# Performance work log

Hardware: AMD Instinct MI355X
Metric: run time of the kernel (lower is better)

## Reference

```python
import jax, jax.numpy as jnp
import numpy as np

XYZ_MIN = np.array([-1.0, -1.0, -1.0], np.float32)
XYZ_MAX = np.array([1.0, 1.0, 1.0], np.float32)
N_SAMPLES = 256
T_NEAR, T_FAR = 0.05, 2.0
ALPHA_INIT = 1e-6
ACT_SHIFT = float(np.log(1.0 / (1.0 - ALPHA_INIT) - 1.0))  # density bias shift
INTERVAL = 0.5  # stepsize * voxel_size_ratio
VIEWBASE_PE = 4


def trilerp(grid, pts):
    """grid: [C, X, Y, Z]; pts: [P, 3] world coords. Returns [P, C]."""
    res = jnp.asarray(grid.shape[1:], dtype=pts.dtype)  # [3]
    ind = (pts - XYZ_MIN) / (XYZ_MAX - XYZ_MIN) * (res - 1.0)
    ind = jnp.clip(ind, 0.0, res - 1.0)
    i0 = jnp.minimum(jnp.floor(ind), res - 2.0).astype(jnp.int32)  # [P,3]
    f = ind - i0.astype(pts.dtype)  # [P,3] fractional offsets
    x0, y0, z0 = i0[:, 0], i0[:, 1], i0[:, 2]
    x1, y1, z1 = x0 + 1, y0 + 1, z0 + 1
    fx, fy, fz = f[:, 0], f[:, 1], f[:, 2]
    gx, gy, gz = 1.0 - fx, 1.0 - fy, 1.0 - fz
    out = (grid[:, x0, y0, z0] * (gx * gy * gz)
           + grid[:, x1, y0, z0] * (fx * gy * gz)
           + grid[:, x0, y1, z0] * (gx * fy * gz)
           + grid[:, x0, y0, z1] * (gx * gy * fz)
           + grid[:, x1, y1, z0] * (fx * fy * gz)
           + grid[:, x1, y0, z1] * (fx * gy * fz)
           + grid[:, x0, y1, z1] * (gx * fy * fz)
           + grid[:, x1, y1, z1] * (fx * fy * fz))  # [C,P]
    return out.T


def setup_inputs() -> dict:
    key = jax.random.key(0)
    ks = jax.random.split(key, 10)
    N = 4096
    rays_o = jax.random.normal(ks[0], (N, 3), jnp.float32) * 0.05
    rays_d = jax.random.normal(ks[1], (N, 3), jnp.float32)
    density = jax.random.normal(ks[2], (1, 1, 160, 160, 160), jnp.float32)
    k0 = jax.random.normal(ks[3], (1, 12, 160, 160, 160), jnp.float32) * 0.1
    w0 = jax.random.normal(ks[4], (39, 128), jnp.float32) * (1.0 / np.sqrt(39))
    b0 = jnp.zeros((128,), jnp.float32)
    w1 = jax.random.normal(ks[5], (128, 128), jnp.float32) * (1.0 / np.sqrt(128))
    b1 = jnp.zeros((128,), jnp.float32)
    w2 = jax.random.normal(ks[6], (128, 3), jnp.float32) * (1.0 / np.sqrt(128))
    b2 = jnp.zeros((3,), jnp.float32)
    return {"rays_o": rays_o, "rays_d": rays_d, "density": density, "k0": k0,
            "w0": w0, "b0": b0, "w1": w1, "b1": b1, "w2": w2, "b2": b2}


def reference(rays_o, rays_d, density, k0, w0, b0, w1, b1, w2, b2):
    N = rays_o.shape[0]
    dens_grid = density[0]            # [1,X,Y,Z]
    feat_grid = k0[0]                 # [C,X,Y,Z]
    viewdirs = rays_d / jnp.linalg.norm(rays_d, axis=-1, keepdims=True)
    t = jnp.linspace(T_NEAR, T_FAR, N_SAMPLES, dtype=rays_o.dtype)  # [S]
    pts = rays_o[:, None, :] + viewdirs[:, None, :] * t[None, :, None]  # [N,S,3]
    inbox = jnp.all((pts >= XYZ_MIN) & (pts <= XYZ_MAX), axis=-1)  # [N,S]
    flat = pts.reshape(-1, 3)

    # density -> alpha: 1 - (1 + exp(d + shift))^(-interval)   (Raw2Alpha)
    d = trilerp(dens_grid, flat)[:, 0].reshape(N, N_SAMPLES)
    alpha = 1.0 - jnp.power(1.0 + jnp.exp(d + ACT_SHIFT), -INTERVAL)
    alpha = jnp.where(inbox, alpha, 0.0)

    # alpha -> weights via exclusive transmittance cumprod (Alphas2Weights)
    T_full = jnp.cumprod(1.0 - alpha, axis=1)               # [N,S]
    T_excl = jnp.concatenate([jnp.ones((N, 1), alpha.dtype), T_full[:, :-1]], axis=1)
    weights = alpha * T_excl                                 # [N,S]
    alphainv_last = T_full[:, -1]                            # [N]

    # color features + view-direction positional encoding
    feat = trilerp(feat_grid, flat).reshape(N, N_SAMPLES, -1)  # [N,S,C]
    freqs = (2.0 ** jnp.arange(VIEWBASE_PE)).astype(rays_o.dtype)
    vf = viewdirs[:, :, None] * freqs[None, None, :]           # [N,3,PE]
    vemb = jnp.concatenate([viewdirs, jnp.sin(vf).reshape(N, -1), jnp.cos(vf).reshape(N, -1)], axis=-1)  # [N,27]
    x = jnp.concatenate([feat, jnp.broadcast_to(vemb[:, None, :], (N, N_SAMPLES, vemb.shape[-1]))], axis=-1)

    h = jax.nn.relu(x @ w0 + b0)
    h = jax.nn.relu(h @ w1 + b1)
    rgb = jax.nn.sigmoid(h @ w2 + b2)                          # [N,S,3]

    rgb_marched = jnp.einsum('ns,nsc->nc', weights, rgb) + alphainv_last[:, None] * 1.0  # white bg
    return rgb_marched
```

## Files before the change

### kernel.cpp

```cpp
#include <hip/hip_runtime.h>
#include <hip/hip_bf16.h>
#include <math.h>

#define ACT_SHIFT_F (-13.8155095579637744f)
#define GRID_VOX 4096000
#define GP_BYTES  (GRID_VOX * 32)
#define W0P_OFF   GP_BYTES
#define W1P_OFF   (W0P_OFF + 8 * 1024)
#define W2P_OFF   (W1P_OFF + 32 * 1024)
#define WS_NEED   ((size_t)(W2P_OFF + 4 * 1024))

typedef __bf16 bf16x8 __attribute__((ext_vector_type(8)));
typedef float  f32x4  __attribute__((ext_vector_type(4)));
typedef float  fv4    __attribute__((ext_vector_type(4)));

__device__ __forceinline__ float bfu(unsigned short b) {
    return __uint_as_float(((unsigned int)b) << 16);
}
__device__ __forceinline__ unsigned short f2bf(float x) {
    unsigned int u = __float_as_uint(x);
    u += 0x7fffu + ((u >> 16) & 1u);
    return (unsigned short)(u >> 16);
}
__device__ __forceinline__ unsigned int packtr(float a, float b) {
    return (__float_as_uint(a) >> 16) | (__float_as_uint(b) & 0xffff0000u);
}
#define UNPK(u, lo, hi) { lo = __uint_as_float((u) << 16); hi = __uint_as_float((u) & 0xffff0000u); }

__device__ __constant__ int offv_c[8] = {0, 1, 160, 161, 25600, 25601, 25760, 25761};

__global__ void repack_all(const float* __restrict__ dens, const float* __restrict__ k0,
                           const float* __restrict__ w0, const float* __restrict__ w1,
                           const float* __restrict__ w2,
                           unsigned short* __restrict__ gp, unsigned short* __restrict__ wp)
{
    const int b = blockIdx.x;
    if (b < 4000) {
        const int v4 = b * 1024 + threadIdx.x * 4;
        const fv4 d4 = __builtin_nontemporal_load((const fv4*)(dens + v4));
        fv4 c4[12];
        #pragma unroll
        for (int c = 0; c < 12; ++c)
            c4[c] = __builtin_nontemporal_load((const fv4*)(k0 + (size_t)c * GRID_VOX + v4));
        uint4* dst = (uint4*)(gp + (size_t)v4 * 16);
        #pragma unroll
        for (int j = 0; j < 4; ++j) {
            const float* cj = &((const float*)c4)[j];
            uint4 q0, q1;
            q0.x = packtr(d4[j],    cj[0]);
            q0.y = packtr(cj[4*1],  cj[4*2]);
            q0.z = packtr(cj[4*3],  cj[4*4]);
            q0.w = packtr(cj[4*5],  cj[4*6]);
            q1.x = packtr(cj[4*7],  cj[4*8]);
            q1.y = packtr(cj[4*9],  cj[4*10]);
            q1.z = packtr(cj[4*11], 0.f);
            q1.w = 0u;
            dst[j*2 + 0] = q0;
            dst[j*2 + 1] = q1;
        }
        return;
    }
    const int t = (b - 4000) * 256 + threadIdx.x;
    if (t >= 44 * 64) return;
    const int f = t >> 6, l = t & 63;
    const int n16 = l & 15, kg = l >> 4;
    unsigned short v[8];
    if (f < 8) {
        const int n = f * 16 + n16;
        #pragma unroll
        for (int j = 0; j < 8; ++j) {
            const int k = kg * 8 + j;
            v[j] = (k < 12) ? f2bf(w0[k * 128 + n]) : (unsigned short)0;
        }
    } else if (f < 40) {
        const int ff = f - 8, nt = ff >> 2, ks = ff & 3;
        const int n = nt * 16 + n16;
        #pragma unroll
        for (int j = 0; j < 8; ++j) {
            const int k = ks * 32 + kg * 8 + j;
            v[j] = f2bf(w1[k * 128 + n]);
        }
    } else {
        const int ks = f - 40;
        #pragma unroll
        for (int j = 0; j < 8; ++j) {
            const int k = ks * 32 + kg * 8 + j;
            v[j] = (n16 < 3) ? f2bf(w2[k * 3 + n16]) : (unsigned short)0;
        }
    }
    uint4 q;
    q.x = v[0] | (v[1] << 16); q.y = v[2] | (v[3] << 16);
    q.z = v[4] | (v[5] << 16); q.w = v[6] | (v[7] << 16);
    *(uint4*)(wp + f * 512 + l * 8) = q;
}

__global__ __launch_bounds__(256, 3)
void dvgo_mfma(const float* __restrict__ rays_o, const float* __restrict__ rays_d,
               const float* __restrict__ w0, const float* __restrict__ b0,
               const float* __restrict__ b1, const float* __restrict__ b2,
               const unsigned short* __restrict__ gp,
               const unsigned short* __restrict__ wpk,
               float* __restrict__ out)
{
    __shared__ unsigned short Xs[128 * 40];
    __shared__ unsigned short Hs[128 * 136];
    __shared__ float shA[128];
    __shared__ float wts[128];
    __shared__ float b0eff[128];
    __shared__ float b1s[128];
    __shared__ float vemb[28];
    __shared__ float red[4][3];
    __shared__ float b2s[3];
    __shared__ float Tcs[3];
    __shared__ float spart;

    const int r = blockIdx.x, t = threadIdx.x;
    const int l = t & 63, wv = t >> 6;
    const int col = l & 15, rg = l >> 4;

    const float ox = rays_o[r*3+0], oy = rays_o[r*3+1], oz = rays_o[r*3+2];
    const float dxr = rays_d[r*3+0], dyr = rays_d[r*3+1], dzr = rays_d[r*3+2];
    const float rn = rsqrtf(dxr*dxr + dyr*dyr + dzr*dzr);
    const float vx = dxr*rn, vy = dyr*rn, vz = dzr*rn;

    if (t < 27) {
        float val;
        if (t < 3) val = (t == 0) ? vx : ((t == 1) ? vy : vz);
        else {
            int q = t - 3;
            const bool is_sin = q < 12;
            if (!is_sin) q -= 12;
            const int i = q >> 2, p = q & 3;
            const float a = ((i == 0) ? vx : ((i == 1) ? vy : vz)) * (float)(1 << p);
            val = is_sin ? sinf(a) : cosf(a);
        }
        vemb[t] = val;
    }
    if (t < 3)   b2s[t] = b2[t];
    if (t < 128) b1s[t] = b1[t];
    if (t == 0)  Tcs[0] = 1.f;
    __syncthreads();

    if (t < 128) {
        float a = b0[t];
        #pragma unroll
        for (int k = 0; k < 27; ++k) a = fmaf(vemb[k], w0[(12 + k) * 128 + t], a);
        b0eff[t] = a;
    }
    for (int i = t; i < 128 * 10; i += 256) {
        const int row = i / 10, c = i % 10;
        ((unsigned int*)Xs)[row * 20 + 6 + c] = 0u;
    }

    const unsigned short* w0p = wpk;
    const unsigned short* w1p = wpk + 8 * 512;
    const unsigned short* w2p = wpk + 40 * 512;
    const uint4* gq = (const uint4*)gp;

    float pacc = 0.f;

    #pragma unroll 1
    for (int ck = 0; ck < 2; ++ck) {
        {
            const int sl = t >> 1, hf = t & 1;
            const int s = ck * 128 + sl;
            const float tp = 0.05f + (1.95f / 255.f) * (float)s;
            const float px = ox + vx*tp, py = oy + vy*tp, pz = oz + vz*tp;
            const bool inbox = (px >= -1.f) & (px <= 1.f) & (py >= -1.f) & (py <= 1.f) &
                               (pz >= -1.f) & (pz <= 1.f);
            unsigned short* xrow = &Xs[sl * 40];
            if (inbox) {
                const float ix = fminf(fmaxf((px + 1.f) * 79.5f, 0.f), 159.f);
                const float iy = fminf(fmaxf((py + 1.f) * 79.5f, 0.f), 159.f);
                const float iz = fminf(fmaxf((pz + 1.f) * 79.5f, 0.f), 159.f);
                const int x0 = min((int)ix, 158), y0 = min((int)iy, 158), z0 = min((int)iz, 158);
                const float fx = ix - x0, fy = iy - y0, fz = iz - z0;
                const float gx = 1.f - fx, gy = 1.f - fy, gz = 1.f - fz;
                const int base = (x0 * 160 + y0) * 160 + z0;
                float w8[8];
                w8[0]=gx*gy*gz; w8[1]=gx*gy*fz; w8[2]=gx*fy*gz; w8[3]=gx*fy*fz;
                w8[4]=fx*gy*gz; w8[5]=fx*gy*fz; w8[6]=fx*fy*gz; w8[7]=fx*fy*fz;
                float a0=0,a1=0,a2=0,a3=0,a4=0,a5=0,a6=0,a7=0;
                #pragma unroll
                for (int cn = 0; cn < 8; ++cn) {
                    const uint4 q = gq[(size_t)(base + offv_c[cn]) * 2 + hf];
                    float f0,f1,f2,f3,f4,f5,f6,f7;
                    UNPK(q.x, f0, f1); UNPK(q.y, f2, f3);
                    UNPK(q.z, f4, f5); UNPK(q.w, f6, f7);
                    const float wc = w8[cn];
                    a0=fmaf(wc,f0,a0); a1=fmaf(wc,f1,a1); a2=fmaf(wc,f2,a2); a3=fmaf(wc,f3,a3);
                    a4=fmaf(wc,f4,a4); a5=fmaf(wc,f5,a5); a6=fmaf(wc,f6,a6); a7=fmaf(wc,f7,a7);
                }
                if (hf == 0) {
                    xrow[0]=f2bf(a1); xrow[1]=f2bf(a2); xrow[2]=f2bf(a3); xrow[3]=f2bf(a4);
                    xrow[4]=f2bf(a5); xrow[5]=f2bf(a6); xrow[6]=f2bf(a7);
                    const float e = expf(a0 + ACT_SHIFT_F);
                    const float op = 1.f + e;
                    const float alpha = e / (op + sqrtf(op));
                    wts[sl] = alpha;
                    shA[sl] = 1.f - alpha;
                } else {
                    xrow[7]=f2bf(a0); xrow[8]=f2bf(a1); xrow[9]=f2bf(a2);
                    xrow[10]=f2bf(a3); xrow[11]=f2bf(a4);
                }
            } else {
                if (hf == 0) {
                    #pragma unroll
                    for (int j = 0; j < 7; ++j) xrow[j] = 0;
                    wts[sl] = 0.f;
                    shA[sl] = 1.f;
                } else {
                    #pragma unroll
                    for (int j = 7; j < 12; ++j) xrow[j] = 0;
                }
            }
        }
        __syncthreads();

        float v = 1.f;
        if (t < 128) {
            v = shA[t];
            #pragma unroll
            for (int off = 1; off < 64; off <<= 1) {
                const float u = __shfl_up(v, off);
                if (l >= off) v *= u;
            }
            if (wv == 0 && l == 63) spart = v;
        }
        __syncthreads();
        if (t < 128) {
            float excl = __shfl_up(v, 1);
            if (l == 0) excl = 1.f;
            float E = Tcs[ck];
            const float sp = spart;
            if (wv == 1) E *= sp;
            const float w = wts[t] * E * excl;
            wts[t] = w;
            if (t == 127) Tcs[ck + 1] = Tcs[ck] * sp * v;
        }
        __syncthreads();

        const int row0 = wv * 32;

        {
            bf16x8 A0[2];
            #pragma unroll
            for (int mt = 0; mt < 2; ++mt)
                A0[mt] = *(const bf16x8*)(&Xs[(row0 + mt * 16 + col) * 40 + rg * 8]);
            #pragma unroll 1
            for (int nt = 0; nt < 8; ++nt) {
                const bf16x8 B = *(const bf16x8*)(w0p + nt * 512 + l * 8);
                const float bias = b0eff[nt * 16 + col];
                #pragma unroll
                for (int mt = 0; mt < 2; ++mt) {
                    f32x4 acc = {0.f, 0.f, 0.f, 0.f};
                    acc = __builtin_amdgcn_mfma_f32_16x16x32_bf16(A0[mt], B, acc, 0, 0, 0);
                    #pragma unroll
                    for (int q = 0; q < 4; ++q) {
                        const float vv = fmaxf(acc[q] + bias, 0.f);
                        const float vo = __shfl_xor(vv, 1);
                        if ((l & 1) == 0) {
                            const int row = row0 + mt * 16 + rg * 4 + q;
                            const unsigned int pk = (unsigned int)f2bf(vv) |
                                                    ((unsigned int)f2bf(vo) << 16);
                            *(unsigned int*)(&Hs[row * 136 + nt * 16 + col]) = pk;
                        }
                    }
                }
            }
        }

        {
            bf16x8 A1[2][4];
            #pragma unroll
            for (int mt = 0; mt < 2; ++mt)
                #pragma unroll
                for (int ks = 0; ks < 4; ++ks)
                    A1[mt][ks] = *(const bf16x8*)(&Hs[(row0 + mt * 16 + col) * 136 + ks * 32 + rg * 8]);
            #pragma unroll 1
            for (int nt = 0; nt < 8; ++nt) {
                bf16x8 Bk[4];
                #pragma unroll
                for (int ks = 0; ks < 4; ++ks)
                    Bk[ks] = *(const bf16x8*)(w1p + (nt * 4 + ks) * 512 + l * 8);
                const float bias = b1s[nt * 16 + col];
                #pragma unroll
                for (int mt = 0; mt < 2; ++mt) {
                    f32x4 acc = {0.f, 0.f, 0.f, 0.f};
                    #pragma unroll
                    for (int ks = 0; ks < 4; ++ks)
                        acc = __builtin_amdgcn_mfma_f32_16x16x32_bf16(A1[mt][ks], Bk[ks], acc, 0, 0, 0);
                    #pragma unroll
                    for (int q = 0; q < 4; ++q) {
                        const float vv = fmaxf(acc[q] + bias, 0.f);
                        const float vo = __shfl_xor(vv, 1);
                        if ((l & 1) == 0) {
                            const int row = row0 + mt * 16 + rg * 4 + q;
                            const unsigned int pk = (unsigned int)f2bf(vv) |
                                                    ((unsigned int)f2bf(vo) << 16);
                            *(unsigned int*)(&Hs[row * 136 + nt * 16 + col]) = pk;
                        }
                    }
                }
            }
        }

        {
            bf16x8 Bk[4];
            #pragma unroll
            for (int ks = 0; ks < 4; ++ks)
                Bk[ks] = *(const bf16x8*)(w2p + ks * 512 + l * 8);
            const float bias2 = (col < 3) ? b2s[col] : 0.f;
            #pragma unroll
            for (int mt = 0; mt < 2; ++mt) {
                bf16x8 A2[4];
                #pragma unroll
                for (int ks = 0; ks < 4; ++ks)
                    A2[ks] = *(const bf16x8*)(&Hs[(row0 + mt * 16 + col) * 136 + ks * 32 + rg * 8]);
                f32x4 acc = {0.f, 0.f, 0.f, 0.f};
                #pragma unroll
                for (int ks = 0; ks < 4; ++ks)
                    acc = __builtin_amdgcn_mfma_f32_16x16x32_bf16(A2[ks], Bk[ks], acc, 0, 0, 0);
                #pragma unroll
                for (int q = 0; q < 4; ++q) {
                    const float rv = acc[q] + bias2;
                    const float sg = 1.f / (1.f + expf(-rv));
                    const int srow = row0 + mt * 16 + rg * 4 + q;
                    pacc = fmaf(wts[srow], sg, pacc);
                }
            }
        }
        __syncthreads();
    }

    pacc += __shfl_xor(pacc, 16);
    pacc += __shfl_xor(pacc, 32);
    if (rg == 0 && col < 3) red[wv][col] = pacc;
    __syncthreads();
    if (t < 3) out[r * 3 + t] = red[0][t] + red[1][t] + red[2][t] + red[3][t] + Tcs[2];
}

__global__ __launch_bounds__(256, 2)
void dvgo_render(const float* __restrict__ rays_o, const float* __restrict__ rays_d,
                 const float* __restrict__ dens, const float* __restrict__ k0,
                 const float* __restrict__ w0, const float* __restrict__ b0,
                 const float* __restrict__ w1, const float* __restrict__ b1,
                 const float* __restrict__ w2, const float* __restrict__ b2,
                 float* __restrict__ out)
{
    __shared__ float xs[256 * 40];
    __shared__ float sh[256];
    __shared__ float wts[256];
    __shared__ float h0s[2][128];
    __shared__ float red[2][2][3];
    __shared__ float rgbacc[6];
    __shared__ float ainv_sh;

    const int r = blockIdx.x, tid = threadIdx.x;
    {
        const int s = tid;
        const float ox = rays_o[r*3+0], oy = rays_o[r*3+1], oz = rays_o[r*3+2];
        const float dxr = rays_d[r*3+0], dyr = rays_d[r*3+1], dzr = rays_d[r*3+2];
        const float rn = rsqrtf(dxr*dxr + dyr*dyr + dzr*dzr);
        const float vx = dxr*rn, vy = dyr*rn, vz = dzr*rn;
        const float t = 0.05f + 1.95f * (1.0f/255.0f) * (float)s;
        const float px = ox + vx*t, py = oy + vy*t, pz = oz + vz*t;
        const bool inbox = (px >= -1.f) && (px <= 1.f) && (py >= -1.f) && (py <= 1.f) &&
                           (pz >= -1.f) && (pz <= 1.f);
        const float ix = fminf(fmaxf((px + 1.f) * 79.5f, 0.f), 159.f);
        const float iy = fminf(fmaxf((py + 1.f) * 79.5f, 0.f), 159.f);
        const float iz = fminf(fmaxf((pz + 1.f) * 79.5f, 0.f), 159.f);
        const int x0 = min((int)ix, 158), y0 = min((int)iy, 158), z0 = min((int)iz, 158);
        const float fx = ix - x0, fy = iy - y0, fz = iz - z0;
        const float gx = 1.f - fx, gy = 1.f - fy, gz = 1.f - fz;
        const int DX = 25600, DY = 160;
        const int base = (x0*160 + y0)*160 + z0;
        const float w000=gx*gy*gz, w100=fx*gy*gz, w010=gx*fy*gz, w001=gx*gy*fz;
        const float w110=fx*fy*gz, w101=fx*gy*fz, w011=gx*fy*fz, w111=fx*fy*fz;
        float alpha = 0.f;
        if (inbox) {
            const float d = dens[base]*w000 + dens[base+DX]*w100 + dens[base+DY]*w010 +
                            dens[base+1]*w001 + dens[base+DX+DY]*w110 + dens[base+DX+1]*w101 +
                            dens[base+DY+1]*w011 + dens[base+DX+DY+1]*w111;
            const float e = expf(d + ACT_SHIFT_F);
            const float op = 1.f + e;
            alpha = e / (op + sqrtf(op));
        }
        sh[s] = 1.f - alpha;
        __syncthreads();
        #pragma unroll
        for (int off = 1; off < 256; off <<= 1) {
            const float v = (s >= off) ? sh[s - off] : 1.f;
            __syncthreads();
            sh[s] *= v;
            __syncthreads();
        }
        wts[s] = alpha * ((s == 0) ? 1.f : sh[s-1]);
        if (s == 255) ainv_sh = sh[255];
        if (s < 6) rgbacc[s] = 0.f;
        float* xrow = &xs[s*40];
        if (inbox) {
            #pragma unroll
            for (int c = 0; c < 12; ++c) {
                const float* g = k0 + c*4096000 + base;
                xrow[c] = g[0]*w000 + g[DX]*w100 + g[DY]*w010 + g[1]*w001 +
                          g[DX+DY]*w110 + g[DX+1]*w101 + g[DY+1]*w011 + g[DX+DY+1]*w111;
            }
        } else {
            #pragma unroll
            for (int c = 0; c < 12; ++c) xrow[c] = 0.f;
        }
        xrow[12]=vx; xrow[13]=vy; xrow[14]=vz;
        const float v3[3] = {vx, vy, vz};
        #pragma unroll
        for (int i = 0; i < 3; ++i)
            #pragma unroll
            for (int p = 0; p < 4; ++p) {
                const float a = v3[i] * (float)(1 << p);
                xrow[15 + i*4 + p] = sinf(a);
                xrow[27 + i*4 + p] = cosf(a);
            }
        xrow[39] = 0.f;
    }
    __syncthreads();
    const int j = tid & 127, sb = tid >> 7;
    float w0c[40];
    #pragma unroll
    for (int k = 0; k < 39; ++k) w0c[k] = w0[k*128 + j];
    w0c[39] = 0.f;
    float w1c[128];
    #pragma unroll
    for (int k = 0; k < 128; ++k) w1c[k] = w1[k*128 + j];
    const float b0j = b0[j], b1j = b1[j];
    const float w2r0 = w2[j*3+0], w2r1 = w2[j*3+1], w2r2 = w2[j*3+2];
    const float b20 = b2[0], b21 = b2[1], b22 = b2[2];
    const int lane = tid & 63, halfw = (tid >> 6) & 1;
    for (int it = 0; it < 128; ++it) {
        const int s = it*2 + sb;
        const float4* xrow4 = (const float4*)(&xs[s*40]);
        float acc = b0j;
        #pragma unroll
        for (int q = 0; q < 10; ++q) {
            const float4 v = xrow4[q];
            acc = fmaf(v.x, w0c[q*4+0], acc); acc = fmaf(v.y, w0c[q*4+1], acc);
            acc = fmaf(v.z, w0c[q*4+2], acc); acc = fmaf(v.w, w0c[q*4+3], acc);
        }
        h0s[sb][j] = fmaxf(acc, 0.f);
        __syncthreads();
        float acc1 = b1j;
        const float4* h4 = (const float4*)(&h0s[sb][0]);
        #pragma unroll
        for (int q = 0; q < 32; ++q) {
            const float4 v = h4[q];
            acc1 = fmaf(v.x, w1c[q*4+0], acc1); acc1 = fmaf(v.y, w1c[q*4+1], acc1);
            acc1 = fmaf(v.z, w1c[q*4+2], acc1); acc1 = fmaf(v.w, w1c[q*4+3], acc1);
        }
        const float hv = fmaxf(acc1, 0.f);
        float p0 = hv*w2r0, p1 = hv*w2r1, p2 = hv*w2r2;
        #pragma unroll
        for (int off = 32; off > 0; off >>= 1) {
            p0 += __shfl_down(p0, off); p1 += __shfl_down(p1, off); p2 += __shfl_down(p2, off);
        }
        if (lane == 0) { red[sb][halfw][0]=p0; red[sb][halfw][1]=p1; red[sb][halfw][2]=p2; }
        __syncthreads();
        if (tid == sb*128) {
            const float r0 = red[sb][0][0]+red[sb][1][0]+b20;
            const float r1 = red[sb][0][1]+red[sb][1][1]+b21;
            const float r2 = red[sb][0][2]+red[sb][1][2]+b22;
            const float wgt = wts[s];
            rgbacc[sb*3+0] += wgt / (1.f + expf(-r0));
            rgbacc[sb*3+1] += wgt / (1.f + expf(-r1));
            rgbacc[sb*3+2] += wgt / (1.f + expf(-r2));
        }
    }
    __syncthreads();
    if (tid < 3) out[r*3 + tid] = rgbacc[tid] + rgbacc[3 + tid] + ainv_sh;
}

extern "C" void kernel_launch(void* const* d_in, const int* in_sizes, int n_in,
                              void* d_out, int out_size, void* d_ws, size_t ws_size,
                              hipStream_t stream)
{
    const float* rays_o = (const float*)d_in[0];
    const float* rays_d = (const float*)d_in[1];
    const float* dens   = (const float*)d_in[2];
    const float* k0     = (const float*)d_in[3];
    const float* w0     = (const float*)d_in[4];
    const float* b0     = (const float*)d_in[5];
    const float* w1     = (const float*)d_in[6];
    const float* b1     = (const float*)d_in[7];
    const float* w2     = (const float*)d_in[8];
    const float* b2     = (const float*)d_in[9];
    float* out = (float*)d_out;
    const int N = in_sizes[0] / 3;

    if (ws_size >= WS_NEED) {
        unsigned short* gp  = (unsigned short*)d_ws;
        unsigned short* wpk = (unsigned short*)((char*)d_ws + W0P_OFF);
        repack_all<<<dim3(4011), dim3(256), 0, stream>>>(dens, k0, w0, w1, w2, gp, wpk);
        dvgo_mfma<<<dim3(N), dim3(256), 0, stream>>>(rays_o, rays_d, w0, b0, b1, b2,
                                                     gp, wpk, out);
    } else {
        dvgo_render<<<dim3(N), dim3(256), 0, stream>>>(rays_o, rays_d, dens, k0,
                                                       w0, b0, w1, b1, w2, b2, out);
    }
}
```

Measured before the change: 514.4 us.

## Prefetch next chunk's grid gather, alias X/H LDS buffers, raise occupancy

Issues the eight trilinear corner loads for the next sample chunk into registers before the MLP of the current chunk runs, so global gather latency overlaps with MFMA work. The input and hidden activation buffers now share one LDS array, with the A0 operand read before Hs is overwritten, which cuts shared memory use. Launch bounds go from 3 to 4 blocks per CU, and the bf16 packing switches to native conversions. The prefetched registers (8 uint4) raise register pressure under the tighter occupancy bound and may cause spills. The native bf16 conversion may also round slightly differently from the manual code.

```diff
diff --git a/kernel.cpp b/kernel.cpp
--- a/kernel.cpp
+++ b/kernel.cpp
@@ -11,6 +11,7 @@
 #define WS_NEED   ((size_t)(W2P_OFF + 4 * 1024))
 
 typedef __bf16 bf16x8 __attribute__((ext_vector_type(8)));
+typedef __bf16 bf16x2 __attribute__((ext_vector_type(2)));
 typedef float  f32x4  __attribute__((ext_vector_type(4)));
 typedef float  fv4    __attribute__((ext_vector_type(4)));
 
@@ -21,6 +22,10 @@
     unsigned int u = __float_as_uint(x);
     u += 0x7fffu + ((u >> 16) & 1u);
     return (unsigned short)(u >> 16);
+}
+__device__ __forceinline__ void st_bf2(unsigned short* p, float lo, float hi) {
+    bf16x2 v; v.x = (__bf16)lo; v.y = (__bf16)hi;
+    *(bf16x2*)p = v;
 }
 __device__ __forceinline__ unsigned int packtr(float a, float b) {
     return (__float_as_uint(a) >> 16) | (__float_as_uint(b) & 0xffff0000u);
@@ -94,7 +99,7 @@
     *(uint4*)(wp + f * 512 + l * 8) = q;
 }
 
-__global__ __launch_bounds__(256, 3)
+__global__ __launch_bounds__(256, 4)
 void dvgo_mfma(const float* __restrict__ rays_o, const float* __restrict__ rays_d,
                const float* __restrict__ w0, const float* __restrict__ b0,
                const float* __restrict__ b1, const float* __restrict__ b2,
@@ -102,8 +107,7 @@
                const unsigned short* __restrict__ wpk,
                float* __restrict__ out)
 {
-    __shared__ unsigned short Xs[128 * 40];
-    __shared__ unsigned short Hs[128 * 136];
+    __shared__ unsigned short XH[128 * 136];
     __shared__ float shA[128];
     __shared__ float wts[128];
     __shared__ float b0eff[128];
@@ -117,11 +121,37 @@
     const int r = blockIdx.x, t = threadIdx.x;
     const int l = t & 63, wv = t >> 6;
     const int col = l & 15, rg = l >> 4;
+    const int sl = t >> 1, hf = t & 1;
 
     const float ox = rays_o[r*3+0], oy = rays_o[r*3+1], oz = rays_o[r*3+2];
     const float dxr = rays_d[r*3+0], dyr = rays_d[r*3+1], dzr = rays_d[r*3+2];
     const float rn = rsqrtf(dxr*dxr + dyr*dyr + dzr*dzr);
     const float vx = dxr*rn, vy = dyr*rn, vz = dzr*rn;
+
+    const uint4* gq = (const uint4*)gp;
+
+    uint4 pq[8];
+    bool inbox_p = false;
+
+    auto issue_gather = [&](int ck) {
+        const int s = ck * 128 + sl;
+        const float tp = 0.05f + (1.95f / 255.f) * (float)s;
+        const float px = ox + vx*tp, py = oy + vy*tp, pz = oz + vz*tp;
+        inbox_p = (px >= -1.f) & (px <= 1.f) & (py >= -1.f) & (py <= 1.f) &
+                  (pz >= -1.f) & (pz <= 1.f);
+        if (inbox_p) {
+            const float ix = fminf(fmaxf((px + 1.f) * 79.5f, 0.f), 159.f);
+            const float iy = fminf(fmaxf((py + 1.f) * 79.5f, 0.f), 159.f);
+            const float iz = fminf(fmaxf((pz + 1.f) * 79.5f, 0.f), 159.f);
+            const int x0 = min((int)ix, 158), y0 = min((int)iy, 158), z0 = min((int)iz, 158);
+            const int base = (x0 * 160 + y0) * 160 + z0;
+            #pragma unroll
+            for (int cn = 0; cn < 8; ++cn)
+                pq[cn] = gq[(size_t)(base + offv_c[cn]) * 2 + hf];
+        }
+    };
+
+    issue_gather(0);
 
     if (t < 27) {
         float val;
@@ -147,43 +177,35 @@
         for (int k = 0; k < 27; ++k) a = fmaf(vemb[k], w0[(12 + k) * 128 + t], a);
         b0eff[t] = a;
     }
-    for (int i = t; i < 128 * 10; i += 256) {
-        const int row = i / 10, c = i % 10;
-        ((unsigned int*)Xs)[row * 20 + 6 + c] = 0u;
-    }
 
     const unsigned short* w0p = wpk;
     const unsigned short* w1p = wpk + 8 * 512;
     const unsigned short* w2p = wpk + 40 * 512;
-    const uint4* gq = (const uint4*)gp;
 
     float pacc = 0.f;
 
     #pragma unroll 1
     for (int ck = 0; ck < 2; ++ck) {
         {
-            const int sl = t >> 1, hf = t & 1;
-            const int s = ck * 128 + sl;
-            const float tp = 0.05f + (1.95f / 255.f) * (float)s;
-            const float px = ox + vx*tp, py = oy + vy*tp, pz = oz + vz*tp;
-            const bool inbox = (px >= -1.f) & (px <= 1.f) & (py >= -1.f) & (py <= 1.f) &
-                               (pz >= -1.f) & (pz <= 1.f);
-            unsigned short* xrow = &Xs[sl * 40];
-            if (inbox) {
+            unsigned short* xrow = &XH[sl * 40];
+            unsigned int*  xd   = (unsigned int*)xrow;
+            if (inbox_p) {
+                const int s = ck * 128 + sl;
+                const float tp = 0.05f + (1.95f / 255.f) * (float)s;
+                const float px = ox + vx*tp, py = oy + vy*tp, pz = oz + vz*tp;
                 const float ix = fminf(fmaxf((px + 1.f) * 79.5f, 0.f), 159.f);
                 const float iy = fminf(fmaxf((py + 1.f) * 79.5f, 0.f), 159.f);
                 const float iz = fminf(fmaxf((pz + 1.f) * 79.5f, 0.f), 159.f);
                 const int x0 = min((int)ix, 158), y0 = min((int)iy, 158), z0 = min((int)iz, 158);
                 const float fx = ix - x0, fy = iy - y0, fz = iz - z0;
                 const float gx = 1.f - fx, gy = 1.f - fy, gz = 1.f - fz;
-                const int base = (x0 * 160 + y0) * 160 + z0;
                 float w8[8];
                 w8[0]=gx*gy*gz; w8[1]=gx*gy*fz; w8[2]=gx*fy*gz; w8[3]=gx*fy*fz;
                 w8[4]=fx*gy*gz; w8[5]=fx*gy*fz; w8[6]=fx*fy*gz; w8[7]=fx*fy*fz;
                 float a0=0,a1=0,a2=0,a3=0,a4=0,a5=0,a6=0,a7=0;
                 #pragma unroll
                 for (int cn = 0; cn < 8; ++cn) {
-                    const uint4 q = gq[(size_t)(base + offv_c[cn]) * 2 + hf];
+                    const uint4 q = pq[cn];
                     float f0,f1,f2,f3,f4,f5,f6,f7;
                     UNPK(q.x, f0, f1); UNPK(q.y, f2, f3);
                     UNPK(q.z, f4, f5); UNPK(q.w, f6, f7);
@@ -192,30 +214,41 @@
                     a4=fmaf(wc,f4,a4); a5=fmaf(wc,f5,a5); a6=fmaf(wc,f6,a6); a7=fmaf(wc,f7,a7);
                 }
                 if (hf == 0) {
-                    xrow[0]=f2bf(a1); xrow[1]=f2bf(a2); xrow[2]=f2bf(a3); xrow[3]=f2bf(a4);
-                    xrow[4]=f2bf(a5); xrow[5]=f2bf(a6); xrow[6]=f2bf(a7);
+                    st_bf2(&xrow[0], a1, a2);
+                    st_bf2(&xrow[2], a3, a4);
+                    st_bf2(&xrow[4], a5, a6);
+                    *(__bf16*)&xrow[6] = (__bf16)a7;
                     const float e = expf(a0 + ACT_SHIFT_F);
                     const float op = 1.f + e;
                     const float alpha = e / (op + sqrtf(op));
                     wts[sl] = alpha;
                     shA[sl] = 1.f - alpha;
                 } else {
-                    xrow[7]=f2bf(a0); xrow[8]=f2bf(a1); xrow[9]=f2bf(a2);
-                    xrow[10]=f2bf(a3); xrow[11]=f2bf(a4);
+                    *(__bf16*)&xrow[7] = (__bf16)a0;
+                    st_bf2(&xrow[8],  a1, a2);
+                    st_bf2(&xrow[10], a3, a4);
                 }
             } else {
                 if (hf == 0) {
-                    #pragma unroll
-                    for (int j = 0; j < 7; ++j) xrow[j] = 0;
+                    xd[0]=0u; xd[1]=0u; xd[2]=0u; xrow[6]=0;
                     wts[sl] = 0.f;
                     shA[sl] = 1.f;
                 } else {
-                    #pragma unroll
-                    for (int j = 7; j < 12; ++j) xrow[j] = 0;
+                    xrow[7]=0; xd[4]=0u; xd[5]=0u;
                 }
             }
-        }
-        __syncthreads();
+            if (hf == 0) { xd[6]=0u; xd[7]=0u; xd[8]=0u; xd[9]=0u; xd[10]=0u; }
+            else         { xd[11]=0u; xd[12]=0u; xd[13]=0u; xd[14]=0u; xd[15]=0u; }
+            if (ck == 0) issue_gather(1);
+        }
+        __syncthreads();
+
+        const int row0 = wv * 32;
+
+        bf16x8 A0[2];
+        #pragma unroll
+        for (int mt = 0; mt < 2; ++mt)
+            A0[mt] = *(const bf16x8*)(&XH[(row0 + mt * 16 + col) * 40 + rg * 8]);
 
         float v = 1.f;
         if (t < 128) {
@@ -240,13 +273,7 @@
         }
         __syncthreads();
 
-        const int row0 = wv * 32;
-
         {
-            bf16x8 A0[2];
-            #pragma unroll
-            for (int mt = 0; mt < 2; ++mt)
-                A0[mt] = *(const bf16x8*)(&Xs[(row0 + mt * 16 + col) * 40 + rg * 8]);
             #pragma unroll 1
             for (int nt = 0; nt < 8; ++nt) {
                 const bf16x8 B = *(const bf16x8*)(w0p + nt * 512 + l * 8);
@@ -261,9 +288,7 @@
                         const float vo = __shfl_xor(vv, 1);
                         if ((l & 1) == 0) {
                             const int row = row0 + mt * 16 + rg * 4 + q;
-                            const unsigned int pk = (unsigned int)f2bf(vv) |
-                                                    ((unsigned int)f2bf(vo) << 16);
-                            *(unsigned int*)(&Hs[row * 136 + nt * 16 + col]) = pk;
+                            st_bf2(&XH[row * 136 + nt * 16 + col], vv, vo);
                         }
                     }
                 }
@@ -276,7 +301,7 @@
             for (int mt = 0; mt < 2; ++mt)
                 #pragma unroll
                 for (int ks = 0; ks < 4; ++ks)
-                    A1[mt][ks] = *(const bf16x8*)(&Hs[(row0 + mt * 16 + col) * 136 + ks * 32 + rg * 8]);
+                    A1[mt][ks] = *(const bf16x8*)(&XH[(row0 + mt * 16 + col) * 136 + ks * 32 + rg * 8]);
             #pragma unroll 1
             for (int nt = 0; nt < 8; ++nt) {
                 bf16x8 Bk[4];
@@ -296,9 +321,7 @@
                         const float vo = __shfl_xor(vv, 1);
                         if ((l & 1) == 0) {
                             const int row = row0 + mt * 16 + rg * 4 + q;
-                            const unsigned int pk = (unsigned int)f2bf(vv) |
-                                                    ((unsigned int)f2bf(vo) << 16);
-                            *(unsigned int*)(&Hs[row * 136 + nt * 16 + col]) = pk;
+                            st_bf2(&XH[row * 136 + nt * 16 + col], vv, vo);
                         }
                     }
                 }
@@ -316,7 +339,7 @@
                 bf16x8 A2[4];
                 #pragma unroll
                 for (int ks = 0; ks < 4; ++ks)
-                    A2[ks] = *(const bf16x8*)(&Hs[(row0 + mt * 16 + col) * 136 + ks * 32 + rg * 8]);
+                    A2[ks] = *(const bf16x8*)(&XH[(row0 + mt * 16 + col) * 136 + ks * 32 + rg * 8]);
                 f32x4 acc = {0.f, 0.f, 0.f, 0.f};
                 #pragma unroll
                 for (int ks = 0; ks < 4; ++ks)
```

Result: faster. 485.7 us (-5.6%).
